# Performance work log

Measured on AMD Instinct MI355X. Metric: run time of the kernel, lower is better.

## Reference

```python
import jax, jax.numpy as jnp
import numpy as np

NUM_CATS = 5
EPS = 1e-6


def setup_inputs() -> dict:
    key = jax.random.key(0)
    k1, k2, k3, k4 = jax.random.split(key, 4)
    B, C, H, W = 64, 3, 256, 256
    restored = jax.random.normal(k1, (B, C, H, W), dtype=jnp.float32)
    clean_patch_1 = jax.random.normal(k2, (B, C, H, W), dtype=jnp.float32)
    un = jax.random.uniform(k3, (B, C, H, W), dtype=jnp.float32)
    de_id = jax.random.randint(k4, (B,), 0, NUM_CATS)
    return {"restored": restored, "clean_patch_1": clean_patch_1,
            "de_id": de_id, "un": un}


def _loss(restored, clean, un, de_id):
    B, C, H, W = restored.shape
    E = C * H * W  # elements per sample
    dt = restored.dtype

    onehot = (de_id[:, None] == jnp.arange(NUM_CATS)[None, :])  # [B,5] bool
    m = onehot.astype(dt)                                        # [B,5]
    counts = onehot.sum(0)                                       # [5] int
    nonempty = counts > 0
    safe_counts = jnp.maximum(counts, 1).astype(dt)              # avoid 0-div

    # Per-category mean uncertainty map: un_map[c] = mean_{i: de_id[i]=c} un[i] + eps
    un_sum = jnp.einsum('bk,bchw->kchw', m, un)                  # [5,C,H,W]
    un_map = un_sum / safe_counts[:, None, None, None] + EPS     # [5,C,H,W]
    s = 1.0 / un_map                                             # [5,C,H,W]

    # Per-sample scaled L1 (s gathered by each sample's category)
    absdiff = jnp.abs(clean - restored)                          # [B,C,H,W]
    scaled_sum_per_sample = (absdiff * s[de_id]).sum(axis=(1, 2, 3))  # [B]
    abs_sum_per_sample = absdiff.sum(axis=(1, 2, 3))                  # [B]

    cat_scaled_sum = jnp.einsum('bk,b->k', m, scaled_sum_per_sample)  # [5]
    cat_abs_sum = jnp.einsum('bk,b->k', m, abs_sum_per_sample)        # [5]

    # NOTE: the original code never clears un_hq_list/un_lq_list between
    # categories, so the L1 at category c is the mean over ALL samples from
    # categories 0..c (each scaled by its OWN category's s). Replicate that
    # via cumulative sums/counts over the category axis.
    cum_scaled = jnp.cumsum(cat_scaled_sum)                      # [5]
    cum_elems = jnp.cumsum(counts).astype(dt) * E                # [5]
    cum_l1 = cum_scaled / jnp.maximum(cum_elems, 1.0)            # [5]

    old_loss = jnp.where(nonempty, cat_abs_sum / (safe_counts * E), 0.0)
    un_num = un_map.mean(axis=(1, 2, 3))                         # [5]
    bn = jnp.where(nonempty, 2.0 * jnp.log(un_num), 0.0)
    unc_l1 = jnp.where(nonempty, cum_l1, 0.0)

    cat_losses = unc_l1 + bn                                     # [5]
    num = nonempty.sum().astype(dt)
    total = cat_losses.sum() / num
    return total, cat_losses, old_loss, bn, unc_l1


def reference(restored, clean_patch_1, de_id, un):
    return _loss(restored, clean_patch_1, un, de_id)
```

## Files before the change

### kernel.cpp

```cpp
#include <hip/hip_runtime.h>
#include <math.h>

#define NCAT  5
#define BATCH 64
#define ELEMS 196608
#define HALF_ELEMS 98304
#define NBLK 768
#define TPB  128
#define EPSV 1e-6f

__global__ __launch_bounds__(TPB) void accum_kernel(
    const float2* __restrict__ restored,
    const float2* __restrict__ clean,
    const int*    __restrict__ de_id,
    const float2* __restrict__ un,
    float*        __restrict__ partials)
{
    __shared__ int   sh_de[BATCH];
    __shared__ float sh_inv[NCAT];
    __shared__ float sred[TPB / 64][3 * NCAT];

    const int tid = threadIdx.x;

    if (tid < 64) {
        int k = de_id[tid];
        sh_de[tid] = k;
        #pragma unroll
        for (int j = 0; j < NCAT; ++j) {
            unsigned long long m = __ballot(k == j);
            if (tid == j) {
                int c = __popcll(m);
                sh_inv[j] = 1.0f / (float)(c > 0 ? c : 1);
            }
        }
    }
    __syncthreads();

    float inv_safe[NCAT];
    #pragma unroll
    for (int j = 0; j < NCAT; ++j) inv_safe[j] = sh_inv[j];

    const int gid = blockIdx.x * TPB + tid;
    const float2* rp = restored + gid;
    const float2* cp = clean + gid;
    const float2* up = un + gid;

    float2 un_s[NCAT], ad_s[NCAT];
    #pragma unroll
    for (int j = 0; j < NCAT; ++j) {
        un_s[j].x = un_s[j].y = 0.f;
        ad_s[j].x = ad_s[j].y = 0.f;
    }

    #pragma unroll 8
    for (int b = 0; b < BATCH; ++b) {
        const size_t off = (size_t)b * HALF_ELEMS;
        float2 u = up[off];
        float2 c = cp[off];
        float2 r = rp[off];
        float adx = fabsf(c.x - r.x);
        float ady = fabsf(c.y - r.y);
        int k = sh_de[b];
        #pragma unroll
        for (int j = 0; j < NCAT; ++j) {
            float m = (k == j) ? 1.0f : 0.0f;
            un_s[j].x = fmaf(m, u.x, un_s[j].x);
            un_s[j].y = fmaf(m, u.y, un_s[j].y);
            ad_s[j].x = fmaf(m, adx, ad_s[j].x);
            ad_s[j].y = fmaf(m, ady, ad_s[j].y);
        }
    }

    float vals[3 * NCAT];
    #pragma unroll
    for (int j = 0; j < NCAT; ++j) {
        float umx = fmaf(un_s[j].x, inv_safe[j], EPSV);
        float umy = fmaf(un_s[j].y, inv_safe[j], EPSV);
        vals[j]            = ad_s[j].x / umx + ad_s[j].y / umy;
        vals[NCAT + j]     = ad_s[j].x + ad_s[j].y;
        vals[2 * NCAT + j] = un_s[j].x + un_s[j].y;
    }

    #pragma unroll
    for (int i = 0; i < 3 * NCAT; ++i) {
        float v = vals[i];
        #pragma unroll
        for (int off = 32; off >= 1; off >>= 1)
            v += __shfl_down(v, off, 64);
        vals[i] = v;
    }

    const int wave = tid >> 6;
    const int lane = tid & 63;
    if (lane == 0) {
        #pragma unroll
        for (int i = 0; i < 3 * NCAT; ++i) sred[wave][i] = vals[i];
    }
    __syncthreads();

    if (tid < 3 * NCAT) {
        float v = sred[0][tid] + sred[1][tid];
        partials[tid * NBLK + blockIdx.x] = v;
    }
}

__global__ __launch_bounds__(256) void epilogue_kernel(
    const int*   __restrict__ de_id,
    const float* __restrict__ partials,
    float*       __restrict__ out)
{
    __shared__ int   sh_cnt[NCAT];
    __shared__ float sh_acc[3 * NCAT];

    const int tid = threadIdx.x;

    if (tid < 64) {
        int k = de_id[tid];
        #pragma unroll
        for (int j = 0; j < NCAT; ++j) {
            unsigned long long m = __ballot(k == j);
            if (tid == j) sh_cnt[j] = __popcll(m);
        }
    }

    if (tid < 240) {
        const int row    = tid >> 4;
        const int lane16 = tid & 15;
        float v = 0.f;
        #pragma unroll 4
        for (int k = 0; k < NBLK / 16; ++k)
            v += partials[row * NBLK + lane16 + (k << 4)];
        v += __shfl_down(v, 8, 16);
        v += __shfl_down(v, 4, 16);
        v += __shfl_down(v, 2, 16);
        v += __shfl_down(v, 1, 16);
        if (lane16 == 0) sh_acc[row] = v;
    }
    __syncthreads();

    if (tid == 0) {
        const float Ef = (float)ELEMS;
        float cum_s = 0.f;
        long  cum_c = 0;
        float total = 0.f;
        int   num   = 0;

        float cat_losses[NCAT], old_loss[NCAT], bn[NCAT], unc_l1[NCAT];

        for (int j = 0; j < NCAT; ++j) {
            cum_s += sh_acc[j];
            cum_c += sh_cnt[j];
            float cum_elems = (float)cum_c * Ef;
            float cum_l1    = cum_s / fmaxf(cum_elems, 1.0f);

            bool  ne   = sh_cnt[j] > 0;
            float safe = (float)(ne ? sh_cnt[j] : 1);

            old_loss[j]  = ne ? sh_acc[NCAT + j] / (safe * Ef) : 0.f;
            float un_num = sh_acc[2 * NCAT + j] / (safe * Ef) + EPSV;
            bn[j]        = ne ? 2.0f * logf(un_num) : 0.f;
            unc_l1[j]    = ne ? cum_l1 : 0.f;
            cat_losses[j] = unc_l1[j] + bn[j];
            total += cat_losses[j];
            num   += ne ? 1 : 0;
        }
        total /= (float)num;

        out[0] = total;
        for (int j = 0; j < NCAT; ++j) {
            out[1 + j]  = cat_losses[j];
            out[6 + j]  = old_loss[j];
            out[11 + j] = bn[j];
            out[16 + j] = unc_l1[j];
        }
    }
}

extern "C" void kernel_launch(void* const* d_in, const int* in_sizes, int n_in,
                              void* d_out, int out_size, void* d_ws, size_t ws_size,
                              hipStream_t stream) {
    (void)in_sizes; (void)n_in; (void)out_size; (void)ws_size;
    const float2* restored = (const float2*)d_in[0];
    const float2* clean    = (const float2*)d_in[1];
    const int*    de_id    = (const int*)d_in[2];
    const float2* un       = (const float2*)d_in[3];
    float* out      = (float*)d_out;
    float* partials = (float*)d_ws;

    accum_kernel<<<NBLK, TPB, 0, stream>>>(restored, clean, de_id, un, partials);
    epilogue_kernel<<<1, 256, 0, stream>>>(de_id, partials, out);
}
```

Baseline: 176.2 us.

## Switch to scalar float loads with double-buffered register prefetch across batch groups

Each thread now handles one float per sample instead of a float2, and blocks grow from 128 to 256 threads, so the grid still covers every pixel. The batch loop is split into groups of 8 samples, and the next group's loads are issued into a second register buffer while the current group is accumulated. The aim is to keep more independent loads in flight and hide memory latency in this bandwidth-bound reduction. In exchange, accesses are narrower per load, register pressure rises from the 2x8x3 buffers, and occupancy may drop.

```diff
diff --git a/kernel.cpp b/kernel.cpp
--- a/kernel.cpp
+++ b/kernel.cpp
@@ -4,17 +4,17 @@
 #define NCAT  5
 #define BATCH 64
 #define ELEMS 196608
-#define HALF_ELEMS 98304
-#define NBLK 768
-#define TPB  128
-#define EPSV 1e-6f
+#define NBLK  768
+#define TPB   256
+#define GRP   8
+#define EPSV  1e-6f
 
 __global__ __launch_bounds__(TPB) void accum_kernel(
-    const float2* __restrict__ restored,
-    const float2* __restrict__ clean,
-    const int*    __restrict__ de_id,
-    const float2* __restrict__ un,
-    float*        __restrict__ partials)
+    const float* __restrict__ restored,
+    const float* __restrict__ clean,
+    const int*   __restrict__ de_id,
+    const float* __restrict__ un,
+    float*       __restrict__ partials)
 {
     __shared__ int   sh_de[BATCH];
     __shared__ float sh_inv[NCAT];
@@ -36,49 +36,58 @@
     }
     __syncthreads();
 
-    float inv_safe[NCAT];
-    #pragma unroll
-    for (int j = 0; j < NCAT; ++j) inv_safe[j] = sh_inv[j];
-
-    const int gid = blockIdx.x * TPB + tid;
-    const float2* rp = restored + gid;
-    const float2* cp = clean + gid;
-    const float2* up = un + gid;
-
-    float2 un_s[NCAT], ad_s[NCAT];
+    const int p = blockIdx.x * TPB + tid;
+    const float* rp = restored + p;
+    const float* cp = clean + p;
+    const float* up = un + p;
+
+    float un_s[NCAT] = {0.f, 0.f, 0.f, 0.f, 0.f};
+    float ad_s[NCAT] = {0.f, 0.f, 0.f, 0.f, 0.f};
+
+    float ub[2][GRP], cb[2][GRP], rb[2][GRP];
+
+    #pragma unroll
+    for (int i = 0; i < GRP; ++i) {
+        const size_t off = (size_t)i * ELEMS;
+        ub[0][i] = up[off];
+        cb[0][i] = cp[off];
+        rb[0][i] = rp[off];
+    }
+
+    #pragma unroll
+    for (int g = 0; g < BATCH / GRP; ++g) {
+        const int cur = g & 1;
+        const int nxt = cur ^ 1;
+        if (g < BATCH / GRP - 1) {
+            #pragma unroll
+            for (int i = 0; i < GRP; ++i) {
+                const size_t off = (size_t)((g + 1) * GRP + i) * ELEMS;
+                ub[nxt][i] = up[off];
+                cb[nxt][i] = cp[off];
+                rb[nxt][i] = rp[off];
+            }
+        }
+        #pragma unroll
+        for (int i = 0; i < GRP; ++i) {
+            float u  = ub[cur][i];
+            float ad = fabsf(cb[cur][i] - rb[cur][i]);
+            int   k  = sh_de[g * GRP + i];
+            #pragma unroll
+            for (int j = 0; j < NCAT; ++j) {
+                float m = (k == j) ? 1.0f : 0.0f;
+                un_s[j] = fmaf(m, u,  un_s[j]);
+                ad_s[j] = fmaf(m, ad, ad_s[j]);
+            }
+        }
+    }
+
+    float vals[3 * NCAT];
     #pragma unroll
     for (int j = 0; j < NCAT; ++j) {
-        un_s[j].x = un_s[j].y = 0.f;
-        ad_s[j].x = ad_s[j].y = 0.f;
-    }
-
-    #pragma unroll 8
-    for (int b = 0; b < BATCH; ++b) {
-        const size_t off = (size_t)b * HALF_ELEMS;
-        float2 u = up[off];
-        float2 c = cp[off];
-        float2 r = rp[off];
-        float adx = fabsf(c.x - r.x);
-        float ady = fabsf(c.y - r.y);
-        int k = sh_de[b];
-        #pragma unroll
-        for (int j = 0; j < NCAT; ++j) {
-            float m = (k == j) ? 1.0f : 0.0f;
-            un_s[j].x = fmaf(m, u.x, un_s[j].x);
-            un_s[j].y = fmaf(m, u.y, un_s[j].y);
-            ad_s[j].x = fmaf(m, adx, ad_s[j].x);
-            ad_s[j].y = fmaf(m, ady, ad_s[j].y);
-        }
-    }
-
-    float vals[3 * NCAT];
-    #pragma unroll
-    for (int j = 0; j < NCAT; ++j) {
-        float umx = fmaf(un_s[j].x, inv_safe[j], EPSV);
-        float umy = fmaf(un_s[j].y, inv_safe[j], EPSV);
-        vals[j]            = ad_s[j].x / umx + ad_s[j].y / umy;
-        vals[NCAT + j]     = ad_s[j].x + ad_s[j].y;
-        vals[2 * NCAT + j] = un_s[j].x + un_s[j].y;
+        float um = fmaf(un_s[j], sh_inv[j], EPSV);
+        vals[j]            = ad_s[j] / um;
+        vals[NCAT + j]     = ad_s[j];
+        vals[2 * NCAT + j] = un_s[j];
     }
 
     #pragma unroll
@@ -99,7 +108,7 @@
     __syncthreads();
 
     if (tid < 3 * NCAT) {
-        float v = sred[0][tid] + sred[1][tid];
+        float v = sred[0][tid] + sred[1][tid] + sred[2][tid] + sred[3][tid];
         partials[tid * NBLK + blockIdx.x] = v;
     }
 }
@@ -180,10 +189,10 @@
                               void* d_out, int out_size, void* d_ws, size_t ws_size,
                               hipStream_t stream) {
     (void)in_sizes; (void)n_in; (void)out_size; (void)ws_size;
-    const float2* restored = (const float2*)d_in[0];
-    const float2* clean    = (const float2*)d_in[1];
-    const int*    de_id    = (const int*)d_in[2];
-    const float2* un       = (const float2*)d_in[3];
+    const float* restored = (const float*)d_in[0];
+    const float* clean    = (const float*)d_in[1];
+    const int*   de_id    = (const int*)d_in[2];
+    const float* un       = (const float*)d_in[3];
     float* out      = (float*)d_out;
     float* partials = (float*)d_ws;
 
```

Measured after the change: 173.3 us. No clear change (-1.7%).
